# Optimization experiments

Hardware: AMD Instinct MI355X
Metric: run time of the kernel (lower is better)

## Reference

```python
import jax, jax.numpy as jnp
import numpy as np

AC_KERNEL = 5


def deconv(x, w, stride):
    """torch ConvTranspose2d(k=3, p=1, bias=False), stride 1 or 2 (output_padding=1).
    w has torch layout [Cin, Cout, kH, kW]."""
    wk = jnp.transpose(w, (1, 0, 2, 3))[:, :, ::-1, ::-1]  # OIHW, spatially flipped
    dn = ('NCHW', 'OIHW', 'NCHW')
    if stride == 1:
        return jax.lax.conv_general_dilated(x, wk, (1, 1), ((1, 1), (1, 1)), dimension_numbers=dn)
    # stride 2: dilate input, pad (k-1-p, k-1-p+op) = (1, 2) -> doubles H, W
    return jax.lax.conv_general_dilated(x, wk, (1, 1), ((1, 2), (1, 2)),
                                        lhs_dilation=(2, 2), dimension_numbers=dn)


def sepconv(feat, kv, kh, K):
    """Per-pixel adaptive separable convolution (Niklaus SepConv).
    feat: [B,C,H,W]; kv, kh: [B,K,H,W]. Replication-pad by K//2, then
    out[b,c,y,x] = sum_{i,j} pad[b,c,y+i,x+j] * kv[b,i,y,x] * kh[b,j,y,x]."""
    pad = K // 2
    B, C, H, W = feat.shape
    p = jnp.pad(feat, ((0, 0), (0, 0), (pad, pad), (pad, pad)), mode='edge')
    out = jnp.zeros_like(feat)
    for i in range(K):  # small fixed loop over kernel taps
        row = p[:, :, i:i + H, :]  # [B,C,H,W+2*pad]
        horiz = row[:, :, :, 0:W] * kh[:, 0:1]
        for j in range(1, K):
            horiz = horiz + row[:, :, :, j:j + W] * kh[:, j:j + 1]
        out = out + kv[:, i:i + 1] * horiz
    return out


def fusion(feat, kv, kh, mask):
    tmp = sepconv(feat, kv, kh, AC_KERNEL)
    return mask * tmp + (1.0 - mask) * feat


def setup_inputs() -> dict:
    key = jax.random.key(0)
    ks = jax.random.split(key, 20)
    B, G = 128, 64
    d = {'cont_feat': jax.random.normal(ks[0], (B, G, 8, 8), jnp.float32)}
    sizes = [8, 16, 32, 64]
    for li, s in enumerate(sizes):
        d[f'kv{li}'] = jax.random.uniform(ks[1 + 3 * li], (B, AC_KERNEL, s, s), jnp.float32)
        d[f'kh{li}'] = jax.random.uniform(ks[2 + 3 * li], (B, AC_KERNEL, s, s), jnp.float32)
        d[f'm{li}'] = jax.random.uniform(ks[3 + 3 * li], (B, 1, s, s), jnp.float32)
    wshapes = [(G, G * 8, 3, 3), (G * 8, G * 4, 3, 3), (G * 4, G * 2, 3, 3),
               (G * 2, G * 2, 3, 3), (G * 2, G, 3, 3), (G, 3, 3, 3)]
    for wi, ws in enumerate(wshapes):
        d[f'w{wi + 1}'] = jax.random.normal(ks[13 + wi], ws, jnp.float32) * 0.05
    return d


def reference(cont_feat, kv0, kh0, m0, kv1, kh1, m1, kv2, kh2, m2, kv3, kh3, m3,
              w1, w2, w3, w4, w5, w6):
    # kernel_layer = 4, no_mask = False, use_bn = False
    feat_8 = fusion(cont_feat, kv0, kh0, m0)                      # [B,G,8,8]
    feat_16 = jax.nn.relu(deconv(feat_8, w1, 2))                  # [B,8G,16,16]
    feat_16 = fusion(feat_16, kv1, kh1, m1)
    h = jax.nn.relu(deconv(feat_16, w2, 1))                       # [B,4G,16,16]
    feat_32 = jax.nn.relu(deconv(h, w3, 2))                       # [B,2G,32,32]
    feat_32 = fusion(feat_32, kv2, kh2, m2)
    h = jax.nn.relu(deconv(feat_32, w4, 1))                       # [B,2G,32,32]
    h = jax.nn.relu(deconv(h, w5, 2))                             # [B,G,64,64]
    out = jnp.tanh(deconv(h, w6, 1))                              # [B,3,64,64]
    out = fusion(out, kv3, kh3, m3)
    return (out, feat_8, feat_16, feat_32)
```

## Files before the change

kernel.cpp:

```cpp
#include <hip/hip_runtime.h>
#include <math.h>

typedef short v8s __attribute__((ext_vector_type(8)));
typedef float v16f __attribute__((ext_vector_type(16)));

__device__ inline unsigned short f2bf(float f) {
    union { float f; unsigned u; } c; c.f = f;
    unsigned r = (c.u + 0x7fffu + ((c.u >> 16) & 1u)) >> 16;
    return (unsigned short)r;
}

template<int LW>
__global__ __launch_bounds__(256) void fusion2_kernel(
        const float* __restrict__ feat, const float* __restrict__ kv,
        const float* __restrict__ kh, const float* __restrict__ m,
        float* __restrict__ out, int C, int CH, int H, int lhw) {
    constexpr int W = 1 << LW;
    const int t = blockIdx.x * 256 + threadIdx.x;
    const int hw = H << LW;
    const int b = t >> lhw;
    const int pix = t & (hw - 1);
    const int x = pix & (W - 1);
    const int y = pix >> LW;
    const int lane = threadIdx.x & 63;
    const int rowbase = (lane & ~(W - 1)) << 2;

    const int c0 = blockIdx.y * CH;

    const float mv = m[(size_t)b * hw + pix];
    float kvv[5], khv[5];
#pragma unroll
    for (int i = 0; i < 5; i++) {
        kvv[i] = kv[((size_t)b * 5 + i) * hw + pix];
        khv[i] = kh[((size_t)b * 5 + i) * hw + pix];
    }
    int idx[5];
#pragma unroll
    for (int j = 0; j < 5; j++) {
        int xx = x + j - 2; xx = xx < 0 ? 0 : (xx >= W ? W - 1 : xx);
        idx[j] = rowbase + (xx << 2);
    }
    int roff[5];
#pragma unroll
    for (int i = 0; i < 5; i++) {
        int yy = y + i - 2; yy = yy < 0 ? 0 : (yy >= H ? H - 1 : yy);
        roff[i] = (yy << LW) + x;
    }

    const float* fbase = feat + ((size_t)b * C + c0) * hw;
    float* obase = out + ((size_t)b * C + c0) * hw + pix;
    const float om = 1.f - mv;

#pragma unroll 4
    for (int cc = 0; cc < CH; cc++) {
        const float* q = fbase + (size_t)cc * hw;
        float s = 0.f;
        float fv = 0.f;
#pragma unroll
        for (int i = 0; i < 5; i++) {
            float v = q[roff[i]];
            if (i == 2) fv = v;
            int vb = __float_as_int(v);
            float h = 0.f;
#pragma unroll
            for (int j = 0; j < 5; j++) {
                float nv = __int_as_float(
                    __builtin_amdgcn_ds_bpermute(idx[j], vb));
                h += nv * khv[j];
            }
            s += kvv[i] * h;
        }
        obase[(size_t)cc * hw] = mv * s + om * fv;
    }
}

__global__ __launch_bounds__(256) void nchw_to_nhwc_bf16(
        const float* __restrict__ in, unsigned short* __restrict__ out,
        int C, int H, int W, int lw, int lc2) {
    extern __shared__ unsigned short sm_t[];
    const int y = blockIdx.x, b = blockIdx.y;
    const int Cp = C + 8;
    const int tid = threadIdx.x;
    for (int i = tid; i < C * W; i += 256) {
        int x = i & (W - 1), c = i >> lw;
        float v = in[(((size_t)b * C + c) * H + y) * W + x];
        sm_t[x * Cp + c] = f2bf(v);
    }
    __syncthreads();
    const unsigned* s32 = (const unsigned*)sm_t;
    unsigned* o32 = (unsigned*)(out + (((size_t)b * H + y) * W) * C);
    const int n32 = (W * C) >> 1;
    for (int i = tid; i < n32; i += 256) {
        int x = i >> lc2;
        int c2 = i - (x << lc2);
        o32[i] = s32[x * (Cp >> 1) + c2];
    }
}

__global__ __launch_bounds__(256) void repack_w_frag(
        const float* __restrict__ w, unsigned short* __restrict__ wk,
        int Cin, int Cout, int flip) {
    int idx = blockIdx.x * 256 + threadIdx.x;
    if (idx >= Cin * Cout) return;
    int ci = idx / Cout, co = idx - ci * Cout;
    const float* src = w + (size_t)idx * 9;
    const int nCb = Cout >> 5, nH = Cin >> 4;
    const size_t inner = (size_t)((((ci >> 3) & 1) * 32 + (co & 31)) * 8 + (ci & 7));
#pragma unroll
    for (int k = 0; k < 9; k++) {
        int t = flip ? (8 - k) : k;
        size_t blk = ((size_t)t * nCb + (co >> 5)) * nH + (ci >> 4);
        wk[(blk << 9) + inner] = f2bf(src[k]);
    }
}

template<int W, int TH, int LW>
__global__ __launch_bounds__(256) void conv3x3_mfma(
        const unsigned short* __restrict__ X,
        const unsigned short* __restrict__ Wk,
        unsigned short* __restrict__ out, int Cin, int Cout, int H) {
    constexpr int TP = (TH + 2) * (W + 2);
    constexpr int NIT = TP * 4;
    constexpr int NLD = (NIT + 255) / 256;
    __shared__ unsigned short sB[2][TP * 40];
    const int tid = threadIdx.x;
    const int lane = tid & 63, wv = tid >> 6;
    const int wm = wv >> 1, wn = wv & 1;
    const int y0 = blockIdx.x * TH;
    const int coB = blockIdx.y * 128 + wm * 64;
    const int b = blockIdx.z;
    const int n = lane & 31, kg = lane >> 5;
    const int p0 = wn * 64 + n, p1 = p0 + 32;
    const int r0 = p0 >> LW, c0 = p0 & (W - 1);
    const int r1 = p1 >> LW, c1 = p1 & (W - 1);
    const int bo0 = (r0 * (W + 2) + c0) * 40 + kg * 8;
    const int bo1 = (r1 * (W + 2) + c1) * 40 + kg * 8;
    v16f acc00 = {}, acc01 = {}, acc10 = {}, acc11 = {};
    const size_t cbStride = (size_t)(Cin >> 4) << 9;
    const size_t tStride  = (size_t)(Cout >> 5) * cbStride;
    const unsigned short* Af = Wk + (size_t)(coB >> 5) * cbStride + (lane << 3);
    const unsigned short* Xb = X + (size_t)b * H * W * Cin;

    const unsigned short* ldp[NLD];
    int sto[NLD];
#pragma unroll
    for (int s = 0; s < NLD; s++) {
        int i = tid + s * 256;
        bool slot = (i < NIT);
        int pix = i >> 2, part = i & 3;
        int py = pix / (W + 2), px = pix - py * (W + 2);
        int gy = y0 + py - 1, gx = px - 1;
        bool ok = slot && gy >= 0 && gy < H && (unsigned)gx < (unsigned)W;
        ldp[s] = ok ? Xb + ((size_t)(gy * W + gx)) * Cin + part * 8 : nullptr;
        sto[s] = slot ? pix * 40 + part * 8 : -1;
    }

    uint4 pre[NLD];
#pragma unroll
    for (int s = 0; s < NLD; s++)
        pre[s] = ldp[s] ? *(const uint4*)(ldp[s]) : make_uint4(0u, 0u, 0u, 0u);
#pragma unroll
    for (int s = 0; s < NLD; s++)
        if (sto[s] >= 0) *(uint4*)(sB[0] + sto[s]) = pre[s];
    __syncthreads();

    const int NK = Cin >> 5;
    for (int kk = 0; kk < NK; kk++) {
        const int cur = kk & 1;
        const int ci0 = kk << 5;
        const bool more = (kk + 1 < NK);
        if (more) {
#pragma unroll
            for (int s = 0; s < NLD; s++)
                pre[s] = ldp[s] ? *(const uint4*)(ldp[s] + ci0 + 32)
                                : make_uint4(0u, 0u, 0u, 0u);
        }
        const unsigned short* sC = sB[cur];
#pragma unroll
        for (int t = 0; t < 9; t++) {
            const int ky = t / 3, kx = t - ky * 3;
            const int toff = (ky * (W + 2) + kx) * 40;
#pragma unroll
            for (int kh = 0; kh < 2; kh++) {
                const unsigned short* ap =
                    Af + (size_t)t * tStride + (size_t)(((ci0 >> 4) + kh) << 9);
                v8s A0 = *(const v8s*)(ap);
                v8s A1 = *(const v8s*)(ap + cbStride);
                v8s B0 = *(const v8s*)(sC + bo0 + toff + kh * 16);
                v8s B1 = *(const v8s*)(sC + bo1 + toff + kh * 16);
                acc00 = __builtin_amdgcn_mfma_f32_32x32x16_bf16(A0, B0, acc00, 0, 0, 0);
                acc01 = __builtin_amdgcn_mfma_f32_32x32x16_bf16(A0, B1, acc01, 0, 0, 0);
                acc10 = __builtin_amdgcn_mfma_f32_32x32x16_bf16(A1, B0, acc10, 0, 0, 0);
                acc11 = __builtin_amdgcn_mfma_f32_32x32x16_bf16(A1, B1, acc11, 0, 0, 0);
            }
        }
        if (more) {
            unsigned short* sN = sB[cur ^ 1];
#pragma unroll
            for (int s = 0; s < NLD; s++)
                if (sto[s] >= 0) *(uint4*)(sN + sto[s]) = pre[s];
            __syncthreads();
        }
    }
    unsigned short* ob = out + (size_t)b * H * W * Cout;
#pragma unroll
    for (int sm = 0; sm < 2; sm++) {
        v16f a0 = sm ? acc10 : acc00;
        v16f a1 = sm ? acc11 : acc01;
        const int cobase = coB + sm * 32 + 4 * kg;
        unsigned short* q0p = ob + ((size_t)((y0 + r0) * W + c0)) * Cout + cobase;
        unsigned short* q1p = ob + ((size_t)((y0 + r1) * W + c1)) * Cout + cobase;
#pragma unroll
        for (int r2 = 0; r2 < 4; r2++) {
            ushort4 q0, q1; float v;
            v = a0[4 * r2 + 0]; v = v > 0.f ? v : 0.f; q0.x = f2bf(v);
            v = a0[4 * r2 + 1]; v = v > 0.f ? v : 0.f; q0.y = f2bf(v);
            v = a0[4 * r2 + 2]; v = v > 0.f ? v : 0.f; q0.z = f2bf(v);
            v = a0[4 * r2 + 3]; v = v > 0.f ? v : 0.f; q0.w = f2bf(v);
            *(ushort4*)(q0p + 8 * r2) = q0;
            v = a1[4 * r2 + 0]; v = v > 0.f ? v : 0.f; q1.x = f2bf(v);
            v = a1[4 * r2 + 1]; v = v > 0.f ? v : 0.f; q1.y = f2bf(v);
            v = a1[4 * r2 + 2]; v = v > 0.f ? v : 0.f; q1.z = f2bf(v);
            v = a1[4 * r2 + 3]; v = v > 0.f ? v : 0.f; q1.w = f2bf(v);
            *(ushort4*)(q1p + 8 * r2) = q1;
        }
    }
}

template<int W, int TH, int NWN, int NWM, int LW>
__global__ __launch_bounds__(256) void deconv2_mfma(
        const unsigned short* __restrict__ X,
        const unsigned short* __restrict__ Wk,
        float* __restrict__ out, int Cin, int Cout, int Hin) {
    constexpr int ROWS = NWN * TH + 1;
    constexpr int NPIX = ROWS * (W + 1);
    constexpr int NIT = NPIX * 4;
    constexpr int NLD = (NIT + 255) / 256;
    __shared__ unsigned short sB[2][NPIX * 40];
    const int tid = threadIdx.x;
    const int lane = tid & 63, wv = tid >> 6;
    const int wm = wv / NWN, wn = wv % NWN;
    const int n = lane & 31, kg = lane >> 5;
    const int y0 = blockIdx.x * (NWN * TH);
    const int coB = (blockIdx.y * NWM + wm) * 64;
    const int b = blockIdx.z;
    const int Yl = wn * TH + (n >> LW);
    const int Xl = n & (W - 1);
    v16f zero = {};
    v16f acc[2][2][2];
#pragma unroll
    for (int i = 0; i < 2; i++)
#pragma unroll
        for (int j = 0; j < 2; j++)
#pragma unroll
            for (int s = 0; s < 2; s++) acc[i][j][s] = zero;
    const unsigned short* Xb = X + (size_t)b * Hin * W * Cin;
    const size_t cbStride = (size_t)(Cin >> 4) << 9;
    const size_t tStride  = (size_t)(Cout >> 5) * cbStride;
    const unsigned short* Af = Wk + (size_t)(coB >> 5) * cbStride + (lane << 3);
    const int PY[3] = {1, 0, 1}, DY[3] = {1, 0, 0};

    const unsigned short* ldp[NLD];
    int sto[NLD];
#pragma unroll
    for (int s = 0; s < NLD; s++) {
        int i = tid + s * 256;
        bool slot = (i < NIT);
        int pix = i >> 2, part = i & 3;
        int py_ = pix / (W + 1), px_ = pix - py_ * (W + 1);
        int gy = y0 + py_, gx = px_;
        bool ok = slot && gy < Hin && gx < W;
        ldp[s] = ok ? Xb + ((size_t)(gy * W + gx)) * Cin + part * 8 : nullptr;
        sto[s] = slot ? pix * 40 + part * 8 : -1;
    }

    uint4 pre[NLD];
#pragma unroll
    for (int s = 0; s < NLD; s++)
        pre[s] = ldp[s] ? *(const uint4*)(ldp[s]) : make_uint4(0u, 0u, 0u, 0u);
#pragma unroll
    for (int s = 0; s < NLD; s++)
        if (sto[s] >= 0) *(uint4*)(sB[0] + sto[s]) = pre[s];
    __syncthreads();

    const int NK = Cin >> 5;
    for (int kk = 0; kk < NK; kk++) {
        const int cur = kk & 1;
        const int ci0 = kk << 5;
        const bool more = (kk + 1 < NK);
        if (more) {
#pragma unroll
            for (int s = 0; s < NLD; s++)
                pre[s] = ldp[s] ? *(const uint4*)(ldp[s] + ci0 + 32)
                                : make_uint4(0u, 0u, 0u, 0u);
        }
        const unsigned short* sC = sB[cur];
#pragma unroll
        for (int ky = 0; ky < 3; ky++) {
#pragma unroll
            for (int kx = 0; kx < 3; kx++) {
                const int py = PY[ky], dy = DY[ky];
                const int px = PY[kx], dx = DY[kx];
                const int t = ky * 3 + kx;
                const int boff = ((Yl + dy) * (W + 1) + (Xl + dx)) * 40 + kg * 8;
#pragma unroll
                for (int kh = 0; kh < 2; kh++) {
                    const unsigned short* ap =
                        Af + (size_t)t * tStride + (size_t)(((ci0 >> 4) + kh) << 9);
                    v8s B  = *(const v8s*)(sC + boff + kh * 16);
                    v8s A0 = *(const v8s*)(ap);
                    v8s A1 = *(const v8s*)(ap + cbStride);
                    acc[py][px][0] = __builtin_amdgcn_mfma_f32_32x32x16_bf16(A0, B, acc[py][px][0], 0, 0, 0);
                    acc[py][px][1] = __builtin_amdgcn_mfma_f32_32x32x16_bf16(A1, B, acc[py][px][1], 0, 0, 0);
                }
            }
        }
        if (more) {
            unsigned short* sN = sB[cur ^ 1];
#pragma unroll
            for (int s = 0; s < NLD; s++)
                if (sto[s] >= 0) *(uint4*)(sN + sto[s]) = pre[s];
            __syncthreads();
        }
    }
    const int Wo = 2 * W, Ho = 2 * Hin;
    const int yin = y0 + Yl;
#pragma unroll
    for (int py = 0; py < 2; py++) {
        const int oy = 2 * yin + py;
#pragma unroll
        for (int sm = 0; sm < 2; sm++) {
            const int cobase = coB + sm * 32 + 4 * kg;
#pragma unroll
            for (int r = 0; r < 16; r++) {
                int co = cobase + (r & 3) + 8 * (r >> 2);
                float v0 = acc[py][0][sm][r]; v0 = v0 > 0.f ? v0 : 0.f;
                float v1 = acc[py][1][sm][r]; v1 = v1 > 0.f ? v1 : 0.f;
                *(float2*)(out + (((size_t)(b * Cout + co) * Ho + oy) * Wo + 2 * Xl)) =
                    make_float2(v0, v1);
            }
        }
    }
}

__global__ __launch_bounds__(256) void conv_s1_c3_tanh_kernel(
        const float* __restrict__ in, const float* __restrict__ w,
        float* __restrict__ out, int Cin, int H, int W) {
    __shared__ float sIn[8][18][19];
    __shared__ float sW[8][3][9];
    const int tid = threadIdx.x;
    const int r = tid >> 4, c = tid & 15;
    const int ntx = W >> 4;
    const int tx0 = (blockIdx.x % ntx) << 4, ty0 = (blockIdx.x / ntx) << 4;
    const int b = blockIdx.z;
    const int hw = H * W;
    float acc[3] = {0.f, 0.f, 0.f};
    for (int ci0 = 0; ci0 < Cin; ci0 += 8) {
        for (int i = tid; i < 8 * 18 * 18; i += 256) {
            int ci = i / 324, rr = i % 324, ly = rr / 18, lx = rr % 18;
            int gy = ty0 + ly - 1, gx = tx0 + lx - 1;
            float v = 0.f;
            if (gy >= 0 && gy < H && gx >= 0 && gx < W)
                v = in[(size_t)(b * Cin + ci0 + ci) * hw + gy * W + gx];
            sIn[ci][ly][lx] = v;
        }
        for (int i = tid; i < 8 * 3 * 9; i += 256) {
            int ci = i / 27, rr = i % 27, co = rr / 9, k = rr % 9;
            sW[ci][co][k] = w[(size_t)((ci0 + ci) * 3 + co) * 9 + (8 - k)];
        }
        __syncthreads();
#pragma unroll
        for (int ci = 0; ci < 8; ci++) {
            float v00 = sIn[ci][r][c],     v01 = sIn[ci][r][c + 1],     v02 = sIn[ci][r][c + 2];
            float v10 = sIn[ci][r + 1][c], v11 = sIn[ci][r + 1][c + 1], v12 = sIn[ci][r + 1][c + 2];
            float v20 = sIn[ci][r + 2][c], v21 = sIn[ci][r + 2][c + 1], v22 = sIn[ci][r + 2][c + 2];
#pragma unroll
            for (int co = 0; co < 3; co++) {
                const float* wp = &sW[ci][co][0];
                acc[co] += v00 * wp[0] + v01 * wp[1] + v02 * wp[2]
                         + v10 * wp[3] + v11 * wp[4] + v12 * wp[5]
                         + v20 * wp[6] + v21 * wp[7] + v22 * wp[8];
            }
        }
        __syncthreads();
    }
#pragma unroll
    for (int co = 0; co < 3; co++)
        out[(size_t)(b * 3 + co) * hw + (ty0 + r) * W + tx0 + c] = tanhf(acc[co]);
}

extern "C" void kernel_launch(void* const* d_in, const int* in_sizes, int n_in,
                              void* d_out, int out_size, void* d_ws, size_t ws_size,
                              hipStream_t stream) {
    const float* cont = (const float*)d_in[0];
    const float* kv0 = (const float*)d_in[1];
    const float* kh0 = (const float*)d_in[2];
    const float* m0  = (const float*)d_in[3];
    const float* kv1 = (const float*)d_in[4];
    const float* kh1 = (const float*)d_in[5];
    const float* m1  = (const float*)d_in[6];
    const float* kv2 = (const float*)d_in[7];
    const float* kh2 = (const float*)d_in[8];
    const float* m2  = (const float*)d_in[9];
    const float* kv3 = (const float*)d_in[10];
    const float* kh3 = (const float*)d_in[11];
    const float* m3  = (const float*)d_in[12];
    const float* w1  = (const float*)d_in[13];
    const float* w2  = (const float*)d_in[14];
    const float* w3  = (const float*)d_in[15];
    const float* w4  = (const float*)d_in[16];
    const float* w5  = (const float*)d_in[17];
    const float* w6  = (const float*)d_in[18];

    float* out = (float*)d_out;
    float* f8  = out + 1572864;
    float* f16 = out + 2097152;
    float* f32 = out + 18874368;

    char* ws = (char*)d_ws;

    float* A0 = (float*)ws;
    unsigned short* X8  = (unsigned short*)(ws + 67108864);
    unsigned short* Wk1 = (unsigned short*)(ws + 68157440);

    fusion2_kernel<3><<<dim3(32, 4), 256, 0, stream>>>(
        cont, kv0, kh0, m0, f8, 64, 16, 8, 6);
    nchw_to_nhwc_bf16<<<dim3(8, 128), 256, 8 * 72 * 2, stream>>>(f8, X8, 64, 8, 8, 3, 5);
    repack_w_frag<<<128, 256, 0, stream>>>(w1, Wk1, 64, 512, 0);
    deconv2_mfma<8, 4, 2, 2, 3><<<dim3(1, 4, 128), 256, 0, stream>>>(
        X8, Wk1, A0, 64, 512, 8);
    fusion2_kernel<4><<<dim3(128, 32), 256, 0, stream>>>(
        A0, kv1, kh1, m1, f16, 512, 16, 16, 8);

    unsigned short* X16 = (unsigned short*)ws;
    unsigned short* h1b = (unsigned short*)(ws + 67108864);
    unsigned short* Wk3 = (unsigned short*)(ws + 83886080);
    unsigned short* Wk2 = (unsigned short*)(ws + 84475904);
    nchw_to_nhwc_bf16<<<dim3(16, 128), 256, 16 * 520 * 2, stream>>>(
        f16, X16, 512, 16, 16, 4, 8);
    repack_w_frag<<<512, 256, 0, stream>>>(w2, Wk2, 512, 256, 1);
    conv3x3_mfma<16, 8, 4><<<dim3(2, 2, 128), 256, 0, stream>>>(
        X16, Wk2, h1b, 512, 256, 16);
    repack_w_frag<<<128, 256, 0, stream>>>(w3, Wk3, 256, 128, 0);
    float* t32 = (float*)ws;
    deconv2_mfma<16, 2, 2, 2, 4><<<dim3(4, 1, 128), 256, 0, stream>>>(
        h1b, Wk3, t32, 256, 128, 16);
    fusion2_kernel<5><<<dim3(512, 8), 256, 0, stream>>>(
        t32, kv2, kh2, m2, f32, 128, 16, 32, 10);

    unsigned short* Wk4  = (unsigned short*)ws;
    unsigned short* Wk5  = (unsigned short*)(ws + 294912);
    unsigned short* X32q = (unsigned short*)(ws + 524288);
    unsigned short* h2b  = (unsigned short*)(ws + 8912896);
    float* h3q = (float*)(ws + 17301504);
    float* tq  = (float*)(ws + 50855936);
    repack_w_frag<<<64, 256, 0, stream>>>(w4, Wk4, 128, 128, 1);
    repack_w_frag<<<32, 256, 0, stream>>>(w5, Wk5, 128, 64, 0);
    for (int q = 0; q < 4; q++) {
        size_t bo = (size_t)q * 32;
        const float* f32q = f32 + bo * 128 * 1024;
        nchw_to_nhwc_bf16<<<dim3(32, 32), 256, 32 * 136 * 2, stream>>>(
            f32q, X32q, 128, 32, 32, 5, 6);
        conv3x3_mfma<32, 4, 5><<<dim3(8, 1, 32), 256, 0, stream>>>(
            X32q, Wk4, h2b, 128, 128, 32);
        deconv2_mfma<32, 1, 4, 1, 5><<<dim3(8, 1, 32), 256, 0, stream>>>(
            h2b, Wk5, h3q, 128, 64, 32);
        conv_s1_c3_tanh_kernel<<<dim3(16, 1, 32), 256, 0, stream>>>(h3q, w6, tq, 64, 64, 64);
        fusion2_kernel<6><<<dim3(512, 1), 256, 0, stream>>>(
            tq, kv3 + bo * 5 * 4096, kh3 + bo * 5 * 4096, m3 + bo * 4096,
            out + bo * 3 * 4096, 3, 3, 64, 12);
    }
}
```

Before: 1.045 ms.

## Fuse NHWC bf16 emission into fusion kernels and batch the 32x32 conv

The fusion kernel now also writes its result as packed NHWC bf16 straight into the next convolution's input buffer, so the separate nchw_to_nhwc_bf16 transpose passes at the 8, 16 and 32 resolutions go away. When the workspace is large enough, buffers are rearranged so the 32x32 conv3x3 runs over the whole batch in one launch instead of four quarter-batch launches. Each thread's NHWC store is 16 channels of one pixel, which gives strided uncoalesced writes across a warp. The path also relies on a larger workspace, and the old layout is kept as a fallback.

```diff
diff --git a/kernel.cpp b/kernel.cpp
--- a/kernel.cpp
+++ b/kernel.cpp
@@ -10,11 +10,12 @@
     return (unsigned short)r;
 }
 
-template<int LW>
+template<int LW, int CH>
 __global__ __launch_bounds__(256) void fusion2_kernel(
         const float* __restrict__ feat, const float* __restrict__ kv,
         const float* __restrict__ kh, const float* __restrict__ m,
-        float* __restrict__ out, int C, int CH, int H, int lhw) {
+        float* __restrict__ out, unsigned short* __restrict__ xout,
+        int C, int H, int lhw) {
     constexpr int W = 1 << LW;
     const int t = blockIdx.x * 256 + threadIdx.x;
     const int hw = H << LW;
@@ -51,7 +52,11 @@
     float* obase = out + ((size_t)b * C + c0) * hw + pix;
     const float om = 1.f - mv;
 
-#pragma unroll 4
+    unsigned pk[(CH + 1) / 2];
+#pragma unroll
+    for (int i = 0; i < (CH + 1) / 2; i++) pk[i] = 0u;
+
+#pragma unroll
     for (int cc = 0; cc < CH; cc++) {
         const float* q = fbase + (size_t)cc * hw;
         float s = 0.f;
@@ -70,7 +75,17 @@
             }
             s += kvv[i] * h;
         }
-        obase[(size_t)cc * hw] = mv * s + om * fv;
+        float r = mv * s + om * fv;
+        obase[(size_t)cc * hw] = r;
+        if constexpr (CH == 16)
+            pk[cc >> 1] |= (unsigned)f2bf(r) << ((cc & 1) * 16);
+    }
+    if constexpr (CH == 16) {
+        if (xout) {
+            unsigned short* xp = xout + ((size_t)b * hw + pix) * C + c0;
+            *(uint4*)(xp)     = make_uint4(pk[0], pk[1], pk[2], pk[3]);
+            *(uint4*)(xp + 8) = make_uint4(pk[4], pk[5], pk[6], pk[7]);
+        }
     }
 }
 
@@ -419,55 +434,103 @@
 
     char* ws = (char*)d_ws;
 
-    float* A0 = (float*)ws;
-    unsigned short* X8  = (unsigned short*)(ws + 67108864);
-    unsigned short* Wk1 = (unsigned short*)(ws + 68157440);
-
-    fusion2_kernel<3><<<dim3(32, 4), 256, 0, stream>>>(
-        cont, kv0, kh0, m0, f8, 64, 16, 8, 6);
-    nchw_to_nhwc_bf16<<<dim3(8, 128), 256, 8 * 72 * 2, stream>>>(f8, X8, 64, 8, 8, 3, 5);
-    repack_w_frag<<<128, 256, 0, stream>>>(w1, Wk1, 64, 512, 0);
-    deconv2_mfma<8, 4, 2, 2, 3><<<dim3(1, 4, 128), 256, 0, stream>>>(
-        X8, Wk1, A0, 64, 512, 8);
-    fusion2_kernel<4><<<dim3(128, 32), 256, 0, stream>>>(
-        A0, kv1, kh1, m1, f16, 512, 16, 16, 8);
-
-    unsigned short* X16 = (unsigned short*)ws;
-    unsigned short* h1b = (unsigned short*)(ws + 67108864);
-    unsigned short* Wk3 = (unsigned short*)(ws + 83886080);
-    unsigned short* Wk2 = (unsigned short*)(ws + 84475904);
-    nchw_to_nhwc_bf16<<<dim3(16, 128), 256, 16 * 520 * 2, stream>>>(
-        f16, X16, 512, 16, 16, 4, 8);
-    repack_w_frag<<<512, 256, 0, stream>>>(w2, Wk2, 512, 256, 1);
-    conv3x3_mfma<16, 8, 4><<<dim3(2, 2, 128), 256, 0, stream>>>(
-        X16, Wk2, h1b, 512, 256, 16);
-    repack_w_frag<<<128, 256, 0, stream>>>(w3, Wk3, 256, 128, 0);
-    float* t32 = (float*)ws;
-    deconv2_mfma<16, 2, 2, 2, 4><<<dim3(4, 1, 128), 256, 0, stream>>>(
-        h1b, Wk3, t32, 256, 128, 16);
-    fusion2_kernel<5><<<dim3(512, 8), 256, 0, stream>>>(
-        t32, kv2, kh2, m2, f32, 128, 16, 32, 10);
-
-    unsigned short* Wk4  = (unsigned short*)ws;
-    unsigned short* Wk5  = (unsigned short*)(ws + 294912);
-    unsigned short* X32q = (unsigned short*)(ws + 524288);
-    unsigned short* h2b  = (unsigned short*)(ws + 8912896);
-    float* h3q = (float*)(ws + 17301504);
-    float* tq  = (float*)(ws + 50855936);
-    repack_w_frag<<<64, 256, 0, stream>>>(w4, Wk4, 128, 128, 1);
-    repack_w_frag<<<32, 256, 0, stream>>>(w5, Wk5, 128, 64, 0);
-    for (int q = 0; q < 4; q++) {
-        size_t bo = (size_t)q * 32;
-        const float* f32q = f32 + bo * 128 * 1024;
-        nchw_to_nhwc_bf16<<<dim3(32, 32), 256, 32 * 136 * 2, stream>>>(
-            f32q, X32q, 128, 32, 32, 5, 6);
-        conv3x3_mfma<32, 4, 5><<<dim3(8, 1, 32), 256, 0, stream>>>(
-            X32q, Wk4, h2b, 128, 128, 32);
-        deconv2_mfma<32, 1, 4, 1, 5><<<dim3(8, 1, 32), 256, 0, stream>>>(
-            h2b, Wk5, h3q, 128, 64, 32);
-        conv_s1_c3_tanh_kernel<<<dim3(16, 1, 32), 256, 0, stream>>>(h3q, w6, tq, 64, 64, 64);
-        fusion2_kernel<6><<<dim3(512, 1), 256, 0, stream>>>(
-            tq, kv3 + bo * 5 * 4096, kh3 + bo * 5 * 4096, m3 + bo * 4096,
-            out + bo * 3 * 4096, 3, 3, 64, 12);
-    }
-}
+    if (ws_size >= (size_t)102760448) {
+        float* A0 = (float*)ws;
+        unsigned short* X8  = (unsigned short*)(ws + 67108864);
+        unsigned short* Wk1 = (unsigned short*)(ws + 68157440);
+        unsigned short* X16 = (unsigned short*)(ws + 69206016);
+
+        fusion2_kernel<3, 16><<<dim3(32, 4), 256, 0, stream>>>(
+            cont, kv0, kh0, m0, f8, X8, 64, 8, 6);
+        repack_w_frag<<<128, 256, 0, stream>>>(w1, Wk1, 64, 512, 0);
+        deconv2_mfma<8, 4, 2, 2, 3><<<dim3(1, 4, 128), 256, 0, stream>>>(
+            X8, Wk1, A0, 64, 512, 8);
+        fusion2_kernel<4, 16><<<dim3(128, 32), 256, 0, stream>>>(
+            A0, kv1, kh1, m1, f16, X16, 512, 16, 8);
+
+        unsigned short* h1b = (unsigned short*)ws;
+        unsigned short* Wk2 = (unsigned short*)(ws + 16777216);
+        unsigned short* Wk3 = (unsigned short*)(ws + 19136512);
+        float* t32 = (float*)(ws + 35651584);
+        repack_w_frag<<<512, 256, 0, stream>>>(w2, Wk2, 512, 256, 1);
+        conv3x3_mfma<16, 8, 4><<<dim3(2, 2, 128), 256, 0, stream>>>(
+            X16, Wk2, h1b, 512, 256, 16);
+        repack_w_frag<<<128, 256, 0, stream>>>(w3, Wk3, 256, 128, 0);
+        deconv2_mfma<16, 2, 2, 2, 4><<<dim3(4, 1, 128), 256, 0, stream>>>(
+            h1b, Wk3, t32, 256, 128, 16);
+
+        unsigned short* Wk4 = (unsigned short*)ws;
+        unsigned short* Wk5 = (unsigned short*)(ws + 294912);
+        unsigned short* X32 = (unsigned short*)(ws + 524288);
+        unsigned short* h2b = (unsigned short*)(ws + 35651584);
+        float* h3q = (float*)(ws + 69206016);
+        float* tq  = (float*)(ws + 524288);
+        repack_w_frag<<<64, 256, 0, stream>>>(w4, Wk4, 128, 128, 1);
+        repack_w_frag<<<32, 256, 0, stream>>>(w5, Wk5, 128, 64, 0);
+        fusion2_kernel<5, 16><<<dim3(512, 8), 256, 0, stream>>>(
+            t32, kv2, kh2, m2, f32, X32, 128, 32, 10);
+        conv3x3_mfma<32, 4, 5><<<dim3(8, 1, 128), 256, 0, stream>>>(
+            X32, Wk4, h2b, 128, 128, 32);
+        for (int q = 0; q < 4; q++) {
+            size_t bo = (size_t)q * 32;
+            deconv2_mfma<32, 1, 4, 1, 5><<<dim3(8, 1, 32), 256, 0, stream>>>(
+                h2b + bo * 131072, Wk5, h3q, 128, 64, 32);
+            conv_s1_c3_tanh_kernel<<<dim3(16, 1, 32), 256, 0, stream>>>(h3q, w6, tq, 64, 64, 64);
+            fusion2_kernel<6, 3><<<dim3(512, 1), 256, 0, stream>>>(
+                tq, kv3 + bo * 5 * 4096, kh3 + bo * 5 * 4096, m3 + bo * 4096,
+                out + bo * 3 * 4096, nullptr, 3, 64, 12);
+        }
+    } else {
+        float* A0 = (float*)ws;
+        unsigned short* X8  = (unsigned short*)(ws + 67108864);
+        unsigned short* Wk1 = (unsigned short*)(ws + 68157440);
+
+        fusion2_kernel<3, 16><<<dim3(32, 4), 256, 0, stream>>>(
+            cont, kv0, kh0, m0, f8, nullptr, 64, 8, 6);
+        nchw_to_nhwc_bf16<<<dim3(8, 128), 256, 8 * 72 * 2, stream>>>(f8, X8, 64, 8, 8, 3, 5);
+        repack_w_frag<<<128, 256, 0, stream>>>(w1, Wk1, 64, 512, 0);
+        deconv2_mfma<8, 4, 2, 2, 3><<<dim3(1, 4, 128), 256, 0, stream>>>(
+            X8, Wk1, A0, 64, 512, 8);
+        fusion2_kernel<4, 16><<<dim3(128, 32), 256, 0, stream>>>(
+            A0, kv1, kh1, m1, f16, nullptr, 512, 16, 8);
+
+        unsigned short* X16 = (unsigned short*)ws;
+        unsigned short* h1b = (unsigned short*)(ws + 67108864);
+        unsigned short* Wk3 = (unsigned short*)(ws + 83886080);
+        unsigned short* Wk2 = (unsigned short*)(ws + 84475904);
+        nchw_to_nhwc_bf16<<<dim3(16, 128), 256, 16 * 520 * 2, stream>>>(
+            f16, X16, 512, 16, 16, 4, 8);
+        repack_w_frag<<<512, 256, 0, stream>>>(w2, Wk2, 512, 256, 1);
+        conv3x3_mfma<16, 8, 4><<<dim3(2, 2, 128), 256, 0, stream>>>(
+            X16, Wk2, h1b, 512, 256, 16);
+        repack_w_frag<<<128, 256, 0, stream>>>(w3, Wk3, 256, 128, 0);
+        float* t32 = (float*)ws;
+        deconv2_mfma<16, 2, 2, 2, 4><<<dim3(4, 1, 128), 256, 0, stream>>>(
+            h1b, Wk3, t32, 256, 128, 16);
+        fusion2_kernel<5, 16><<<dim3(512, 8), 256, 0, stream>>>(
+            t32, kv2, kh2, m2, f32, nullptr, 128, 32, 10);
+
+        unsigned short* Wk4  = (unsigned short*)ws;
+        unsigned short* Wk5  = (unsigned short*)(ws + 294912);
+        unsigned short* X32q = (unsigned short*)(ws + 524288);
+        unsigned short* h2b  = (unsigned short*)(ws + 8912896);
+        float* h3q = (float*)(ws + 17301504);
+        float* tq  = (float*)(ws + 50855936);
+        repack_w_frag<<<64, 256, 0, stream>>>(w4, Wk4, 128, 128, 1);
+        repack_w_frag<<<32, 256, 0, stream>>>(w5, Wk5, 128, 64, 0);
+        for (int q = 0; q < 4; q++) {
+            size_t bo = (size_t)q * 32;
+            const float* f32q = f32 + bo * 128 * 1024;
+            nchw_to_nhwc_bf16<<<dim3(32, 32), 256, 32 * 136 * 2, stream>>>(
+                f32q, X32q, 128, 32, 32, 5, 6);
+            conv3x3_mfma<32, 4, 5><<<dim3(8, 1, 32), 256, 0, stream>>>(
+                X32q, Wk4, h2b, 128, 128, 32);
+            deconv2_mfma<32, 1, 4, 1, 5><<<dim3(8, 1, 32), 256, 0, stream>>>(
+                h2b, Wk5, h3q, 128, 64, 32);
+            conv_s1_c3_tanh_kernel<<<dim3(16, 1, 32), 256, 0, stream>>>(h3q, w6, tq, 64, 64, 64);
+            fusion2_kernel<6, 3><<<dim3(512, 1), 256, 0, stream>>>(
+                tq, kv3 + bo * 5 * 4096, kh3 + bo * 5 * 4096, m3 + bo * 4096,
+                out + bo * 3 * 4096, nullptr, 3, 64, 12);
+        }
+    }
+}
```

Result: faster. 933.8 us (-10.7%).
